# Kernel optimization log

Measured on AMD Instinct MI355X. Metric: run time of the kernel, lower is better.

Reference implementation:

```python
import jax, jax.numpy as jnp
import numpy as np

E, T, D, N_RBF, N_SBF = 262144, 1048576, 128, 6, 42


def setup_inputs() -> dict:
    key = jax.random.key(0)
    ks = jax.random.split(key, 24)
    s = 0.05
    inp = {
        "m_ji": jax.random.normal(ks[0], (E, D), jnp.float32),
        "e_rbf": jax.random.normal(ks[1], (E, N_RBF), jnp.float32),
        "a_sbf": jax.random.normal(ks[2], (T, N_SBF), jnp.float32),
        "nbr_list": jax.random.randint(ks[3], (E, 2), 0, 65536),
        "kj_idx": jax.random.randint(ks[4], (T,), 0, E),
        "ji_idx": jax.random.randint(ks[5], (T,), 0, E),
        # edge branch params
        "We": jax.random.normal(ks[6], (N_RBF, D), jnp.float32) * s,
        "W_e1": jax.random.normal(ks[7], (D, D), jnp.float32) * s,
        "b_e1": jnp.zeros((D,), jnp.float32),
        "W_e2": jax.random.normal(ks[8], (D, D), jnp.float32) * s,
        "b_e2": jnp.zeros((D,), jnp.float32),
        "W_e3": jax.random.normal(ks[9], (D, D), jnp.float32) * s,
        "b_e3": jnp.zeros((D,), jnp.float32),
        "W_e4": jax.random.normal(ks[10], (D, D), jnp.float32) * s,
        # angle branch params
        "Wa": jax.random.normal(ks[11], (N_SBF, D), jnp.float32) * s,
        "W_a1": jax.random.normal(ks[12], (D, D), jnp.float32) * s,
        "b_a1": jnp.zeros((D,), jnp.float32),
        "W_a2": jax.random.normal(ks[13], (D, D), jnp.float32) * s,
        "b_a2": jnp.zeros((D,), jnp.float32),
        "W_a3": jax.random.normal(ks[14], (D, D), jnp.float32) * s,
        "b_a3": jnp.zeros((D,), jnp.float32),
        "W_a4": jax.random.normal(ks[15], (D, D), jnp.float32) * s,
    }
    return inp


def _mlp(x, W1, b1, W2, b2, W3, b3, W4):
    x = jax.nn.silu(x @ W1 + b1)
    x = jax.nn.silu(x @ W2 + b2)
    x = jax.nn.silu(x @ W3 + b3)
    return x @ W4


def reference(m_ji, e_rbf, a_sbf, nbr_list, kj_idx, ji_idx,
              We, W_e1, b_e1, W_e2, b_e2, W_e3, b_e3, W_e4,
              Wa, W_a1, b_a1, W_a2, b_a2, W_a3, b_a3, W_a4):
    # edge branch: project rbf to embed dim, gate by edge messages  [E, D]
    edge_feats = _mlp((e_rbf @ We) * m_ji, W_e1, b_e1, W_e2, b_e2, W_e3, b_e3, W_e4)
    # angle branch: project sbf, gate by triplet-gathered message sum  [T, D]
    angle_gate = m_ji[kj_idx] + m_ji[ji_idx]
    angle_feats = _mlp((a_sbf @ Wa) * angle_gate, W_a1, b_a1, W_a2, b_a2, W_a3, b_a3, W_a4)
    return (edge_feats, angle_feats)
```

## Files before the change

kernel.cpp:

```cpp
#include <hip/hip_runtime.h>
#include <stdint.h>

typedef __attribute__((ext_vector_type(8))) short bf16x8;
typedef __attribute__((ext_vector_type(4))) float f32x4;
typedef __attribute__((ext_vector_type(8))) unsigned short us8;

static __device__ __forceinline__ unsigned short f2bf_u(float f) {
  __bf16 h = (__bf16)f;
  return __builtin_bit_cast(unsigned short, h);
}
static __device__ __forceinline__ uint32_t pack2bf(float a, float b) {
  return (uint32_t)f2bf_u(a) | ((uint32_t)f2bf_u(b) << 16);
}
static __device__ __forceinline__ float silu_f(float v) {
  float e = __builtin_amdgcn_exp2f(v * -1.44269504088896341f);
  return v * __builtin_amdgcn_rcpf(1.0f + e);
}

template<bool LAST>
static __device__ __forceinline__ void xlayer(
    const char* __restrict__ src, char* __restrict__ dst,
    const bf16x8* wf, const float* __restrict__ bias,
    float* __restrict__ gout, int l15, int q, int w, int rs)
{
  f32x4 bv;
  if (!LAST) bv = *(const f32x4*)(bias + w * 16 + q * 4);
  #pragma unroll
  for (int rg = 0; rg < 8; ++rg) {
    const int row = rg * 16 + l15;
    f32x4 acc = {0.f, 0.f, 0.f, 0.f};
    #pragma unroll
    for (int ks = 0; ks < 4; ++ks) {
      bf16x8 xf = *(const bf16x8*)(src + ((row * 256 + ks * 64 + q * 16) ^ rs));
      acc = __builtin_amdgcn_mfma_f32_16x16x32_bf16(wf[ks], xf, acc, 0, 0, 0);
    }
    if (!LAST) {
      float v0 = silu_f(acc[0] + bv[0]);
      float v1 = silu_f(acc[1] + bv[1]);
      float v2 = silu_f(acc[2] + bv[2]);
      float v3 = silu_f(acc[3] + bv[3]);
      uint2 u; u.x = pack2bf(v0, v1); u.y = pack2bf(v2, v3);
      *(uint2*)(dst + ((row * 256 + w * 32 + q * 8) ^ rs)) = u;
    } else {
      __builtin_nontemporal_store(acc,
          (f32x4*)(gout + (size_t)row * 128 + w * 16 + q * 4));
    }
  }
}

__global__ __launch_bounds__(512, 4) void angle_kernel(
    const float* __restrict__ m_ji, const float* __restrict__ a_sbf,
    const int* __restrict__ kj, const int* __restrict__ ji,
    const float* __restrict__ b1, const float* __restrict__ b2,
    const float* __restrict__ b3,
    const char* __restrict__ wt4, const char* __restrict__ waT,
    float* __restrict__ out)
{
  extern __shared__ char lds[];
  char* xbA = lds;
  char* xbB = lds + 32768;
  char* aux = lds + 65536;
  const int tid = threadIdx.x, lane = tid & 63, w = tid >> 6;
  const int l15 = lane & 15, q = lane >> 4;
  const int rs = (l15 & 7) << 4;
  const size_t tb = (size_t)blockIdx.x * 128;

  bf16x8 wa0 = *(const bf16x8*)(waT + (w * 2 + 0) * 1024 + lane * 16);
  bf16x8 wa1 = *(const bf16x8*)(waT + (w * 2 + 1) * 1024 + lane * 16);

  int ikj[8], iji[8];
  #pragma unroll
  for (int i2 = 0; i2 < 8; ++i2) {
    ikj[i2] = kj[tb + i2 * 16 + l15];
    iji[i2] = ji[tb + i2 * 16 + l15];
  }

  {
    const float* src = a_sbf + tb * 42;
    #pragma unroll
    for (int j2 = 0; j2 < 8; ++j2) {
      const int i = tid + j2 * 512;
      const int row = i >> 5, p = i & 31;
      const float* rp = src + row * 42 + p * 2;
      float v0 = (p * 2 < 42) ? __builtin_nontemporal_load(rp) : 0.f;
      float v1 = (p * 2 + 1 < 42) ? __builtin_nontemporal_load(rp + 1) : 0.f;
      *(uint32_t*)(aux + ((row * 128 + p * 4) ^ ((row & 7) << 4))) = pack2bf(v0, v1);
    }
  }
  __syncthreads();

  {
    f32x4 pk[8], pj[8];
    auto gissue = [&](int g) {
      pk[g] = *(const f32x4*)(m_ji + (size_t)ikj[g] * 128 + w * 16 + q * 4);
      pj[g] = *(const f32x4*)(m_ji + (size_t)iji[g] * 128 + w * 16 + q * 4);
    };
    gissue(0); gissue(1);
    #pragma unroll
    for (int rg = 0; rg < 8; ++rg) {
      if (rg < 6) gissue(rg + 2);
      const int row = rg * 16 + l15;
      bf16x8 x0f = *(const bf16x8*)(aux + ((row * 128 + q * 16) ^ rs));
      bf16x8 x1f = *(const bf16x8*)(aux + ((row * 128 + 64 + q * 16) ^ rs));
      f32x4 acc = {0.f, 0.f, 0.f, 0.f};
      acc = __builtin_amdgcn_mfma_f32_16x16x32_bf16(wa0, x0f, acc, 0, 0, 0);
      acc = __builtin_amdgcn_mfma_f32_16x16x32_bf16(wa1, x1f, acc, 0, 0, 0);
      f32x4 g = pk[rg] + pj[rg];
      uint2 u;
      u.x = pack2bf(acc[0] * g[0], acc[1] * g[1]);
      u.y = pack2bf(acc[2] * g[2], acc[3] * g[3]);
      *(uint2*)(xbA + ((row * 256 + w * 32 + q * 8) ^ rs)) = u;
    }
  }
  __syncthreads();

  bf16x8 wfl[4][4];
  #pragma unroll
  for (int L = 0; L < 4; ++L)
    #pragma unroll
    for (int ks = 0; ks < 4; ++ks)
      wfl[L][ks] = *(const bf16x8*)(wt4 + L * 32768 + (w * 4 + ks) * 1024 + lane * 16);

  xlayer<false>(xbA, xbB, wfl[0], b1, nullptr, l15, q, w, rs);
  __syncthreads();
  xlayer<false>(xbB, xbA, wfl[1], b2, nullptr, l15, q, w, rs);
  __syncthreads();
  xlayer<false>(xbA, xbB, wfl[2], b3, nullptr, l15, q, w, rs);
  __syncthreads();
  xlayer<true>(xbB, nullptr, wfl[3], nullptr, out + tb * 128, l15, q, w, rs);
}

__global__ __launch_bounds__(512, 4) void edge_kernel(
    const float* __restrict__ m_ji, const float* __restrict__ e_rbf,
    const float* __restrict__ b1, const float* __restrict__ b2,
    const float* __restrict__ b3,
    const char* __restrict__ wt4, const char* __restrict__ weT,
    float* __restrict__ out)
{
  extern __shared__ char lds[];
  char* xbA = lds;
  char* xbB = lds + 32768;
  float* auxF = (float*)(lds + 65536);
  const int tid = threadIdx.x, lane = tid & 63, w = tid >> 6;
  const int l15 = lane & 15, q = lane >> 4;
  const int rs = (l15 & 7) << 4;
  const size_t tb = (size_t)blockIdx.x * 128;

  bf16x8 we = *(const bf16x8*)(weT + w * 1024 + lane * 16);

  {
    const float* src = e_rbf + tb * 6;
    auxF[tid] = __builtin_nontemporal_load(src + tid);
    const int i2 = tid + 512;
    if (i2 < 768) auxF[i2] = __builtin_nontemporal_load(src + i2);
  }
  __syncthreads();

  {
    f32x4 mr[8];
    auto missue = [&](int g) {
      mr[g] = *(const f32x4*)(m_ji + (tb + g * 16 + l15) * 128 + w * 16 + q * 4);
    };
    missue(0); missue(1);
    #pragma unroll
    for (int rg = 0; rg < 8; ++rg) {
      if (rg < 6) missue(rg + 2);
      const int row = rg * 16 + l15;
      bf16x8 ef;
      #pragma unroll
      for (int j = 0; j < 8; ++j) {
        float v = (j < 6) ? auxF[row * 6 + j] : 0.f;
        unsigned short h = (q == 0 && j < 6) ? f2bf_u(v) : (unsigned short)0;
        ef[j] = (short)h;
      }
      f32x4 acc = {0.f, 0.f, 0.f, 0.f};
      acc = __builtin_amdgcn_mfma_f32_16x16x32_bf16(we, ef, acc, 0, 0, 0);
      f32x4 g = mr[rg];
      uint2 u;
      u.x = pack2bf(acc[0] * g[0], acc[1] * g[1]);
      u.y = pack2bf(acc[2] * g[2], acc[3] * g[3]);
      *(uint2*)(xbA + ((row * 256 + w * 32 + q * 8) ^ rs)) = u;
    }
  }
  __syncthreads();

  bf16x8 wfl[4][4];
  #pragma unroll
  for (int L = 0; L < 4; ++L)
    #pragma unroll
    for (int ks = 0; ks < 4; ++ks)
      wfl[L][ks] = *(const bf16x8*)(wt4 + L * 32768 + (w * 4 + ks) * 1024 + lane * 16);

  xlayer<false>(xbA, xbB, wfl[0], b1, nullptr, l15, q, w, rs);
  __syncthreads();
  xlayer<false>(xbB, xbA, wfl[1], b2, nullptr, l15, q, w, rs);
  __syncthreads();
  xlayer<false>(xbA, xbB, wfl[2], b3, nullptr, l15, q, w, rs);
  __syncthreads();
  xlayer<true>(xbB, nullptr, wfl[3], nullptr, out + tb * 128, l15, q, w, rs);
}

__global__ void prep_kernel(
    const float* __restrict__ W0, const float* __restrict__ W1,
    const float* __restrict__ W2, const float* __restrict__ W3,
    const float* __restrict__ W4, const float* __restrict__ W5,
    const float* __restrict__ W6, const float* __restrict__ W7,
    const float* __restrict__ Wa, const float* __restrict__ We,
    char* __restrict__ ws)
{
  const int gid = blockIdx.x * 256 + threadIdx.x;
  const int lane = gid & 63;
  const int l15 = lane & 15, q = lane >> 4;
  if (gid < 16384) {
    const int mat = gid >> 11;
    const int ctks = (gid & 2047) >> 6;
    const int n = (ctks >> 2) * 16 + l15;
    const int k0 = (ctks & 3) * 32 + q * 8;
    const float* W;
    switch (mat) {
      case 0: W = W0; break; case 1: W = W1; break;
      case 2: W = W2; break; case 3: W = W3; break;
      case 4: W = W4; break; case 5: W = W5; break;
      case 6: W = W6; break; default: W = W7; break;
    }
    us8 v;
    #pragma unroll
    for (int j = 0; j < 8; ++j) v[j] = f2bf_u(W[(size_t)(k0 + j) * 128 + n]);
    *(us8*)(ws + mat * 32768 + ctks * 1024 + lane * 16) = v;
  } else if (gid < 17408) {
    const int g = gid - 16384;
    const int ctks = g >> 6;
    const int n = (ctks >> 1) * 16 + l15;
    const int k0 = (ctks & 1) * 32 + q * 8;
    us8 v;
    #pragma unroll
    for (int j = 0; j < 8; ++j) {
      const int k = k0 + j;
      v[j] = (k < 42) ? f2bf_u(Wa[(size_t)k * 128 + n]) : (unsigned short)0;
    }
    *(us8*)(ws + 262144 + ctks * 1024 + lane * 16) = v;
  } else if (gid < 17920) {
    const int g = gid - 17408;
    const int ct = g >> 6;
    const int n = ct * 16 + l15;
    const int k0 = q * 8;
    us8 v;
    #pragma unroll
    for (int j = 0; j < 8; ++j) {
      const int k = k0 + j;
      v[j] = (k < 6) ? f2bf_u(We[(size_t)k * 128 + n]) : (unsigned short)0;
    }
    *(us8*)(ws + 278528 + ct * 1024 + lane * 16) = v;
  }
}

extern "C" void kernel_launch(void* const* d_in, const int* in_sizes, int n_in,
                              void* d_out, int out_size, void* d_ws, size_t ws_size,
                              hipStream_t stream) {
  (void)in_sizes; (void)n_in; (void)out_size; (void)ws_size;
  const float* m_ji  = (const float*)d_in[0];
  const float* e_rbf = (const float*)d_in[1];
  const float* a_sbf = (const float*)d_in[2];
  const int*   kj    = (const int*)d_in[4];
  const int*   ji    = (const int*)d_in[5];
  const float* We    = (const float*)d_in[6];
  const float* We1   = (const float*)d_in[7];
  const float* be1   = (const float*)d_in[8];
  const float* We2   = (const float*)d_in[9];
  const float* be2   = (const float*)d_in[10];
  const float* We3   = (const float*)d_in[11];
  const float* be3   = (const float*)d_in[12];
  const float* We4   = (const float*)d_in[13];
  const float* Wa    = (const float*)d_in[14];
  const float* Wa1   = (const float*)d_in[15];
  const float* ba1   = (const float*)d_in[16];
  const float* Wa2   = (const float*)d_in[17];
  const float* ba2   = (const float*)d_in[18];
  const float* Wa3   = (const float*)d_in[19];
  const float* ba3   = (const float*)d_in[20];
  const float* Wa4   = (const float*)d_in[21];
  char* ws = (char*)d_ws;
  float* out = (float*)d_out;

  hipFuncSetAttribute((const void*)edge_kernel,
                      hipFuncAttributeMaxDynamicSharedMemorySize, 68608);
  hipFuncSetAttribute((const void*)angle_kernel,
                      hipFuncAttributeMaxDynamicSharedMemorySize, 81920);

  prep_kernel<<<70, 256, 0, stream>>>(
      We1, We2, We3, We4, Wa1, Wa2, Wa3, Wa4, Wa, We, ws);
  edge_kernel<<<262144 / 128, 512, 68608, stream>>>(
      m_ji, e_rbf, be1, be2, be3, ws, ws + 278528, out);
  angle_kernel<<<1048576 / 128, 512, 81920, stream>>>(
      m_ji, a_sbf, kj, ji, ba1, ba2, ba3, ws + 131072, ws + 262144,
      out + (size_t)262144 * 128);
}
```

Measured before the change: 632.6 us.

## Shrink blocks to 64 rows with 4 waves each covering 32 output columns

Both MLP kernels now use 256-thread blocks on 64 rows, with each wave computing two 16-column tiles. Weights are loaded per layer instead of all up front, and a_sbf/e_rbf are read straight from global memory into MFMA fragments instead of being staged through LDS. The LDS footprint drops to 32KB static, which should allow more resident blocks and cut register pressure. The cost is more blocks, and a_sbf rows are only 8-byte aligned (42 floats), so the 16-byte vector loads are misaligned.

Result: faster. 525.6 us (-16.9%).

```diff
diff --git a/kernel.cpp b/kernel.cpp
--- a/kernel.cpp
+++ b/kernel.cpp
@@ -5,6 +5,9 @@
 typedef __attribute__((ext_vector_type(4))) float f32x4;
 typedef __attribute__((ext_vector_type(8))) unsigned short us8;
 
+#define T_CNT 1048576
+#define E_CNT 262144
+
 static __device__ __forceinline__ unsigned short f2bf_u(float f) {
   __bf16 h = (__bf16)f;
   return __builtin_bit_cast(unsigned short, h);
@@ -16,39 +19,18 @@
   float e = __builtin_amdgcn_exp2f(v * -1.44269504088896341f);
   return v * __builtin_amdgcn_rcpf(1.0f + e);
 }
-
-template<bool LAST>
-static __device__ __forceinline__ void xlayer(
-    const char* __restrict__ src, char* __restrict__ dst,
-    const bf16x8* wf, const float* __restrict__ bias,
-    float* __restrict__ gout, int l15, int q, int w, int rs)
-{
-  f32x4 bv;
-  if (!LAST) bv = *(const f32x4*)(bias + w * 16 + q * 4);
-  #pragma unroll
-  for (int rg = 0; rg < 8; ++rg) {
-    const int row = rg * 16 + l15;
-    f32x4 acc = {0.f, 0.f, 0.f, 0.f};
-    #pragma unroll
-    for (int ks = 0; ks < 4; ++ks) {
-      bf16x8 xf = *(const bf16x8*)(src + ((row * 256 + ks * 64 + q * 16) ^ rs));
-      acc = __builtin_amdgcn_mfma_f32_16x16x32_bf16(wf[ks], xf, acc, 0, 0, 0);
-    }
-    if (!LAST) {
-      float v0 = silu_f(acc[0] + bv[0]);
-      float v1 = silu_f(acc[1] + bv[1]);
-      float v2 = silu_f(acc[2] + bv[2]);
-      float v3 = silu_f(acc[3] + bv[3]);
-      uint2 u; u.x = pack2bf(v0, v1); u.y = pack2bf(v2, v3);
-      *(uint2*)(dst + ((row * 256 + w * 32 + q * 8) ^ rs)) = u;
-    } else {
-      __builtin_nontemporal_store(acc,
-          (f32x4*)(gout + (size_t)row * 128 + w * 16 + q * 4));
-    }
-  }
-}
-
-__global__ __launch_bounds__(512, 4) void angle_kernel(
+static __device__ __forceinline__ bf16x8 frag8(f32x4 a, f32x4 b) {
+  bf16x8 r;
+  r[0] = (short)f2bf_u(a[0]); r[1] = (short)f2bf_u(a[1]);
+  r[2] = (short)f2bf_u(a[2]); r[3] = (short)f2bf_u(a[3]);
+  r[4] = (short)f2bf_u(b[0]); r[5] = (short)f2bf_u(b[1]);
+  r[6] = (short)f2bf_u(b[2]); r[7] = (short)f2bf_u(b[3]);
+  return r;
+}
+
+__global__ __launch_bounds__(256)
+__attribute__((amdgpu_waves_per_eu(4, 5)))
+void angle_kernel(
     const float* __restrict__ m_ji, const float* __restrict__ a_sbf,
     const int* __restrict__ kj, const int* __restrict__ ji,
     const float* __restrict__ b1, const float* __restrict__ b2,
@@ -56,148 +38,227 @@
     const char* __restrict__ wt4, const char* __restrict__ waT,
     float* __restrict__ out)
 {
-  extern __shared__ char lds[];
-  char* xbA = lds;
-  char* xbB = lds + 32768;
-  char* aux = lds + 65536;
+  __shared__ __align__(16) char xbA[16384];
+  __shared__ __align__(16) char xbB[16384];
   const int tid = threadIdx.x, lane = tid & 63, w = tid >> 6;
   const int l15 = lane & 15, q = lane >> 4;
   const int rs = (l15 & 7) << 4;
-  const size_t tb = (size_t)blockIdx.x * 128;
-
-  bf16x8 wa0 = *(const bf16x8*)(waT + (w * 2 + 0) * 1024 + lane * 16);
-  bf16x8 wa1 = *(const bf16x8*)(waT + (w * 2 + 1) * 1024 + lane * 16);
-
-  int ikj[8], iji[8];
-  #pragma unroll
-  for (int i2 = 0; i2 < 8; ++i2) {
-    ikj[i2] = kj[tb + i2 * 16 + l15];
-    iji[i2] = ji[tb + i2 * 16 + l15];
-  }
-
-  {
-    const float* src = a_sbf + tb * 42;
-    #pragma unroll
-    for (int j2 = 0; j2 < 8; ++j2) {
-      const int i = tid + j2 * 512;
-      const int row = i >> 5, p = i & 31;
-      const float* rp = src + row * 42 + p * 2;
-      float v0 = (p * 2 < 42) ? __builtin_nontemporal_load(rp) : 0.f;
-      float v1 = (p * 2 + 1 < 42) ? __builtin_nontemporal_load(rp + 1) : 0.f;
-      *(uint32_t*)(aux + ((row * 128 + p * 4) ^ ((row & 7) << 4))) = pack2bf(v0, v1);
-    }
+  const size_t tb = (size_t)blockIdx.x * 64;
+  const int cb = w * 32;
+
+  bf16x8 wa[2][2];
+  #pragma unroll
+  for (int ct = 0; ct < 2; ++ct)
+    #pragma unroll
+    for (int ks = 0; ks < 2; ++ks)
+      wa[ct][ks] = *(const bf16x8*)(waT + (((w * 2 + ct) * 2 + ks) << 10) + lane * 16);
+
+  int ikj[4], iji[4];
+  #pragma unroll
+  for (int g = 0; g < 4; ++g) {
+    ikj[g] = kj[tb + g * 16 + l15];
+    iji[g] = ji[tb + g * 16 + l15];
+  }
+
+  f32x4 pk[2][2], pj[2][2];
+  auto gissue = [&](int g) {
+    const float* bk = m_ji + (size_t)ikj[g] * 128 + cb + q * 4;
+    const float* bj = m_ji + (size_t)iji[g] * 128 + cb + q * 4;
+    pk[g & 1][0] = *(const f32x4*)(bk);
+    pk[g & 1][1] = *(const f32x4*)(bk + 16);
+    pj[g & 1][0] = *(const f32x4*)(bj);
+    pj[g & 1][1] = *(const f32x4*)(bj + 16);
+  };
+  gissue(0); gissue(1);
+
+  #pragma unroll
+  for (int rg = 0; rg < 4; ++rg) {
+    const int row = rg * 16 + l15;
+    const float* ap = a_sbf + (tb + row) * 42;
+    f32x4 a0 = *(const f32x4*)(ap + q * 8);
+    f32x4 a1 = *(const f32x4*)(ap + q * 8 + 4);
+    f32x4 c0 = {0.f, 0.f, 0.f, 0.f}, c1 = {0.f, 0.f, 0.f, 0.f};
+    if (q == 0) { c0 = *(const f32x4*)(ap + 32); c1 = *(const f32x4*)(ap + 36); }
+    else if (q == 1) { float2 t = *(const float2*)(ap + 40); c0[0] = t.x; c0[1] = t.y; }
+    bf16x8 f0 = frag8(a0, a1);
+    bf16x8 f1 = frag8(c0, c1);
+    f32x4 acc0 = {0.f, 0.f, 0.f, 0.f}, acc1 = {0.f, 0.f, 0.f, 0.f};
+    acc0 = __builtin_amdgcn_mfma_f32_16x16x32_bf16(wa[0][0], f0, acc0, 0, 0, 0);
+    acc0 = __builtin_amdgcn_mfma_f32_16x16x32_bf16(wa[0][1], f1, acc0, 0, 0, 0);
+    acc1 = __builtin_amdgcn_mfma_f32_16x16x32_bf16(wa[1][0], f0, acc1, 0, 0, 0);
+    acc1 = __builtin_amdgcn_mfma_f32_16x16x32_bf16(wa[1][1], f1, acc1, 0, 0, 0);
+    f32x4 g0 = pk[rg & 1][0] + pj[rg & 1][0];
+    f32x4 g1 = pk[rg & 1][1] + pj[rg & 1][1];
+    if (rg < 2) gissue(rg + 2);
+    uint2 u0, u1;
+    u0.x = pack2bf(acc0[0] * g0[0], acc0[1] * g0[1]);
+    u0.y = pack2bf(acc0[2] * g0[2], acc0[3] * g0[3]);
+    u1.x = pack2bf(acc1[0] * g1[0], acc1[1] * g1[1]);
+    u1.y = pack2bf(acc1[2] * g1[2], acc1[3] * g1[3]);
+    *(uint2*)(xbA + ((row * 256 + w * 64 + q * 8) ^ rs)) = u0;
+    *(uint2*)(xbA + ((row * 256 + w * 64 + 32 + q * 8) ^ rs)) = u1;
   }
   __syncthreads();
 
-  {
-    f32x4 pk[8], pj[8];
-    auto gissue = [&](int g) {
-      pk[g] = *(const f32x4*)(m_ji + (size_t)ikj[g] * 128 + w * 16 + q * 4);
-      pj[g] = *(const f32x4*)(m_ji + (size_t)iji[g] * 128 + w * 16 + q * 4);
-    };
-    gissue(0); gissue(1);
-    #pragma unroll
-    for (int rg = 0; rg < 8; ++rg) {
-      if (rg < 6) gissue(rg + 2);
-      const int row = rg * 16 + l15;
-      bf16x8 x0f = *(const bf16x8*)(aux + ((row * 128 + q * 16) ^ rs));
-      bf16x8 x1f = *(const bf16x8*)(aux + ((row * 128 + 64 + q * 16) ^ rs));
-      f32x4 acc = {0.f, 0.f, 0.f, 0.f};
-      acc = __builtin_amdgcn_mfma_f32_16x16x32_bf16(wa0, x0f, acc, 0, 0, 0);
-      acc = __builtin_amdgcn_mfma_f32_16x16x32_bf16(wa1, x1f, acc, 0, 0, 0);
-      f32x4 g = pk[rg] + pj[rg];
-      uint2 u;
-      u.x = pack2bf(acc[0] * g[0], acc[1] * g[1]);
-      u.y = pack2bf(acc[2] * g[2], acc[3] * g[3]);
-      *(uint2*)(xbA + ((row * 256 + w * 32 + q * 8) ^ rs)) = u;
-    }
-  }
-  __syncthreads();
-
-  bf16x8 wfl[4][4];
-  #pragma unroll
-  for (int L = 0; L < 4; ++L)
-    #pragma unroll
-    for (int ks = 0; ks < 4; ++ks)
-      wfl[L][ks] = *(const bf16x8*)(wt4 + L * 32768 + (w * 4 + ks) * 1024 + lane * 16);
-
-  xlayer<false>(xbA, xbB, wfl[0], b1, nullptr, l15, q, w, rs);
-  __syncthreads();
-  xlayer<false>(xbB, xbA, wfl[1], b2, nullptr, l15, q, w, rs);
-  __syncthreads();
-  xlayer<false>(xbA, xbB, wfl[2], b3, nullptr, l15, q, w, rs);
-  __syncthreads();
-  xlayer<true>(xbB, nullptr, wfl[3], nullptr, out + tb * 128, l15, q, w, rs);
-}
-
-__global__ __launch_bounds__(512, 4) void edge_kernel(
+  #pragma unroll
+  for (int L = 0; L < 4; ++L) {
+    const char* src = (L & 1) ? xbB : xbA;
+    char* dst = (L & 1) ? xbA : xbB;
+    bf16x8 wf[2][4];
+    #pragma unroll
+    for (int ct = 0; ct < 2; ++ct)
+      #pragma unroll
+      for (int ks = 0; ks < 4; ++ks)
+        wf[ct][ks] = *(const bf16x8*)(wt4 + (L << 15) + (((w * 2 + ct) * 4 + ks) << 10) + lane * 16);
+    if (L < 3) {
+      const float* bp = (L == 0) ? b1 : (L == 1) ? b2 : b3;
+      f32x4 bv0 = *(const f32x4*)(bp + cb + q * 4);
+      f32x4 bv1 = *(const f32x4*)(bp + cb + 16 + q * 4);
+      #pragma unroll
+      for (int rg = 0; rg < 4; ++rg) {
+        const int row = rg * 16 + l15;
+        f32x4 acc0 = {0.f, 0.f, 0.f, 0.f}, acc1 = {0.f, 0.f, 0.f, 0.f};
+        #pragma unroll
+        for (int ks = 0; ks < 4; ++ks) {
+          bf16x8 xf = *(const bf16x8*)(src + ((row * 256 + ks * 64 + q * 16) ^ rs));
+          acc0 = __builtin_amdgcn_mfma_f32_16x16x32_bf16(wf[0][ks], xf, acc0, 0, 0, 0);
+          acc1 = __builtin_amdgcn_mfma_f32_16x16x32_bf16(wf[1][ks], xf, acc1, 0, 0, 0);
+        }
+        uint2 u0, u1;
+        u0.x = pack2bf(silu_f(acc0[0] + bv0[0]), silu_f(acc0[1] + bv0[1]));
+        u0.y = pack2bf(silu_f(acc0[2] + bv0[2]), silu_f(acc0[3] + bv0[3]));
+        u1.x = pack2bf(silu_f(acc1[0] + bv1[0]), silu_f(acc1[1] + bv1[1]));
+        u1.y = pack2bf(silu_f(acc1[2] + bv1[2]), silu_f(acc1[3] + bv1[3]));
+        *(uint2*)(dst + ((row * 256 + w * 64 + q * 8) ^ rs)) = u0;
+        *(uint2*)(dst + ((row * 256 + w * 64 + 32 + q * 8) ^ rs)) = u1;
+      }
+      __syncthreads();
+    } else {
+      #pragma unroll
+      for (int rg = 0; rg < 4; ++rg) {
+        const int row = rg * 16 + l15;
+        f32x4 acc0 = {0.f, 0.f, 0.f, 0.f}, acc1 = {0.f, 0.f, 0.f, 0.f};
+        #pragma unroll
+        for (int ks = 0; ks < 4; ++ks) {
+          bf16x8 xf = *(const bf16x8*)(src + ((row * 256 + ks * 64 + q * 16) ^ rs));
+          acc0 = __builtin_amdgcn_mfma_f32_16x16x32_bf16(wf[0][ks], xf, acc0, 0, 0, 0);
+          acc1 = __builtin_amdgcn_mfma_f32_16x16x32_bf16(wf[1][ks], xf, acc1, 0, 0, 0);
+        }
+        float* op = out + (tb + row) * 128 + cb + q * 4;
+        __builtin_nontemporal_store(acc0, (f32x4*)(op));
+        __builtin_nontemporal_store(acc1, (f32x4*)(op + 16));
+      }
+    }
+  }
+}
+
+__global__ __launch_bounds__(256)
+__attribute__((amdgpu_waves_per_eu(4, 5)))
+void edge_kernel(
     const float* __restrict__ m_ji, const float* __restrict__ e_rbf,
     const float* __restrict__ b1, const float* __restrict__ b2,
     const float* __restrict__ b3,
     const char* __restrict__ wt4, const char* __restrict__ weT,
     float* __restrict__ out)
 {
-  extern __shared__ char lds[];
-  char* xbA = lds;
-  char* xbB = lds + 32768;
-  float* auxF = (float*)(lds + 65536);
+  __shared__ __align__(16) char xbA[16384];
+  __shared__ __align__(16) char xbB[16384];
   const int tid = threadIdx.x, lane = tid & 63, w = tid >> 6;
   const int l15 = lane & 15, q = lane >> 4;
   const int rs = (l15 & 7) << 4;
-  const size_t tb = (size_t)blockIdx.x * 128;
-
-  bf16x8 we = *(const bf16x8*)(weT + w * 1024 + lane * 16);
-
-  {
-    const float* src = e_rbf + tb * 6;
-    auxF[tid] = __builtin_nontemporal_load(src + tid);
-    const int i2 = tid + 512;
-    if (i2 < 768) auxF[i2] = __builtin_nontemporal_load(src + i2);
+  const size_t tb = (size_t)blockIdx.x * 64;
+  const int cb = w * 32;
+
+  bf16x8 we[2];
+  #pragma unroll
+  for (int ct = 0; ct < 2; ++ct)
+    we[ct] = *(const bf16x8*)(weT + ((w * 2 + ct) << 10) + lane * 16);
+
+  f32x4 mr[2][2];
+  auto missue = [&](int g) {
+    const float* bm = m_ji + (tb + g * 16 + l15) * 128 + cb + q * 4;
+    mr[g & 1][0] = *(const f32x4*)(bm);
+    mr[g & 1][1] = *(const f32x4*)(bm + 16);
+  };
+  missue(0); missue(1);
+
+  #pragma unroll
+  for (int rg = 0; rg < 4; ++rg) {
+    const int row = rg * 16 + l15;
+    const float* ep = e_rbf + (tb + row) * 6;
+    f32x4 a0 = {0.f, 0.f, 0.f, 0.f}, a1 = {0.f, 0.f, 0.f, 0.f};
+    if (q == 0) {
+      a0 = *(const f32x4*)(ep);
+      float2 t = *(const float2*)(ep + 4);
+      a1[0] = t.x; a1[1] = t.y;
+    }
+    bf16x8 ef = frag8(a0, a1);
+    f32x4 acc0 = {0.f, 0.f, 0.f, 0.f}, acc1 = {0.f, 0.f, 0.f, 0.f};
+    acc0 = __builtin_amdgcn_mfma_f32_16x16x32_bf16(we[0], ef, acc0, 0, 0, 0);
+    acc1 = __builtin_amdgcn_mfma_f32_16x16x32_bf16(we[1], ef, acc1, 0, 0, 0);
+    f32x4 g0 = mr[rg & 1][0];
+    f32x4 g1 = mr[rg & 1][1];
+    if (rg < 2) missue(rg + 2);
+    uint2 u0, u1;
+    u0.x = pack2bf(acc0[0] * g0[0], acc0[1] * g0[1]);
+    u0.y = pack2bf(acc0[2] * g0[2], acc0[3] * g0[3]);
+    u1.x = pack2bf(acc1[0] * g1[0], acc1[1] * g1[1]);
+    u1.y = pack2bf(acc1[2] * g1[2], acc1[3] * g1[3]);
+    *(uint2*)(xbA + ((row * 256 + w * 64 + q * 8) ^ rs)) = u0;
+    *(uint2*)(xbA + ((row * 256 + w * 64 + 32 + q * 8) ^ rs)) = u1;
   }
   __syncthreads();
 
-  {
-    f32x4 mr[8];
-    auto missue = [&](int g) {
-      mr[g] = *(const f32x4*)(m_ji + (tb + g * 16 + l15) * 128 + w * 16 + q * 4);
-    };
-    missue(0); missue(1);
-    #pragma unroll
-    for (int rg = 0; rg < 8; ++rg) {
-      if (rg < 6) missue(rg + 2);
-      const int row = rg * 16 + l15;
-      bf16x8 ef;
-      #pragma unroll
-      for (int j = 0; j < 8; ++j) {
-        float v = (j < 6) ? auxF[row * 6 + j] : 0.f;
-        unsigned short h = (q == 0 && j < 6) ? f2bf_u(v) : (unsigned short)0;
-        ef[j] = (short)h;
+  #pragma unroll
+  for (int L = 0; L < 4; ++L) {
+    const char* src = (L & 1) ? xbB : xbA;
+    char* dst = (L & 1) ? xbA : xbB;
+    bf16x8 wf[2][4];
+    #pragma unroll
+    for (int ct = 0; ct < 2; ++ct)
+      #pragma unroll
+      for (int ks = 0; ks < 4; ++ks)
+        wf[ct][ks] = *(const bf16x8*)(wt4 + (L << 15) + (((w * 2 + ct) * 4 + ks) << 10) + lane * 16);
+    if (L < 3) {
+      const float* bp = (L == 0) ? b1 : (L == 1) ? b2 : b3;
+      f32x4 bv0 = *(const f32x4*)(bp + cb + q * 4);
+      f32x4 bv1 = *(const f32x4*)(bp + cb + 16 + q * 4);
+      #pragma unroll
+      for (int rg = 0; rg < 4; ++rg) {
+        const int row = rg * 16 + l15;
+        f32x4 acc0 = {0.f, 0.f, 0.f, 0.f}, acc1 = {0.f, 0.f, 0.f, 0.f};
+        #pragma unroll
+        for (int ks = 0; ks < 4; ++ks) {
+          bf16x8 xf = *(const bf16x8*)(src + ((row * 256 + ks * 64 + q * 16) ^ rs));
+          acc0 = __builtin_amdgcn_mfma_f32_16x16x32_bf16(wf[0][ks], xf, acc0, 0, 0, 0);
+          acc1 = __builtin_amdgcn_mfma_f32_16x16x32_bf16(wf[1][ks], xf, acc1, 0, 0, 0);
+        }
+        uint2 u0, u1;
+        u0.x = pack2bf(silu_f(acc0[0] + bv0[0]), silu_f(acc0[1] + bv0[1]));
+        u0.y = pack2bf(silu_f(acc0[2] + bv0[2]), silu_f(acc0[3] + bv0[3]));
+        u1.x = pack2bf(silu_f(acc1[0] + bv1[0]), silu_f(acc1[1] + bv1[1]));
+        u1.y = pack2bf(silu_f(acc1[2] + bv1[2]), silu_f(acc1[3] + bv1[3]));
+        *(uint2*)(dst + ((row * 256 + w * 64 + q * 8) ^ rs)) = u0;
+        *(uint2*)(dst + ((row * 256 + w * 64 + 32 + q * 8) ^ rs)) = u1;
       }
-      f32x4 acc = {0.f, 0.f, 0.f, 0.f};
-      acc = __builtin_amdgcn_mfma_f32_16x16x32_bf16(we, ef, acc, 0, 0, 0);
-      f32x4 g = mr[rg];
-      uint2 u;
-      u.x = pack2bf(acc[0] * g[0], acc[1] * g[1]);
-      u.y = pack2bf(acc[2] * g[2], acc[3] * g[3]);
-      *(uint2*)(xbA + ((row * 256 + w * 32 + q * 8) ^ rs)) = u;
-    }
-  }
-  __syncthreads();
-
-  bf16x8 wfl[4][4];
-  #pragma unroll
-  for (int L = 0; L < 4; ++L)
-    #pragma unroll
-    for (int ks = 0; ks < 4; ++ks)
-      wfl[L][ks] = *(const bf16x8*)(wt4 + L * 32768 + (w * 4 + ks) * 1024 + lane * 16);
-
-  xlayer<false>(xbA, xbB, wfl[0], b1, nullptr, l15, q, w, rs);
-  __syncthreads();
-  xlayer<false>(xbB, xbA, wfl[1], b2, nullptr, l15, q, w, rs);
-  __syncthreads();
-  xlayer<false>(xbA, xbB, wfl[2], b3, nullptr, l15, q, w, rs);
-  __syncthreads();
-  xlayer<true>(xbB, nullptr, wfl[3], nullptr, out + tb * 128, l15, q, w, rs);
+      __syncthreads();
+    } else {
+      #pragma unroll
+      for (int rg = 0; rg < 4; ++rg) {
+        const int row = rg * 16 + l15;
+        f32x4 acc0 = {0.f, 0.f, 0.f, 0.f}, acc1 = {0.f, 0.f, 0.f, 0.f};
+        #pragma unroll
+        for (int ks = 0; ks < 4; ++ks) {
+          bf16x8 xf = *(const bf16x8*)(src + ((row * 256 + ks * 64 + q * 16) ^ rs));
+          acc0 = __builtin_amdgcn_mfma_f32_16x16x32_bf16(wf[0][ks], xf, acc0, 0, 0, 0);
+          acc1 = __builtin_amdgcn_mfma_f32_16x16x32_bf16(wf[1][ks], xf, acc1, 0, 0, 0);
+        }
+        float* op = out + (tb + row) * 128 + cb + q * 4;
+        __builtin_nontemporal_store(acc0, (f32x4*)(op));
+        __builtin_nontemporal_store(acc1, (f32x4*)(op + 16));
+      }
+    }
+  }
 }
 
 __global__ void prep_kernel(
@@ -282,16 +343,11 @@
   char* ws = (char*)d_ws;
   float* out = (float*)d_out;
 
-  hipFuncSetAttribute((const void*)edge_kernel,
-                      hipFuncAttributeMaxDynamicSharedMemorySize, 68608);
-  hipFuncSetAttribute((const void*)angle_kernel,
-                      hipFuncAttributeMaxDynamicSharedMemorySize, 81920);
-
   prep_kernel<<<70, 256, 0, stream>>>(
       We1, We2, We3, We4, Wa1, Wa2, Wa3, Wa4, Wa, We, ws);
-  edge_kernel<<<262144 / 128, 512, 68608, stream>>>(
+  edge_kernel<<<E_CNT / 64, 256, 0, stream>>>(
       m_ji, e_rbf, be1, be2, be3, ws, ws + 278528, out);
-  angle_kernel<<<1048576 / 128, 512, 81920, stream>>>(
+  angle_kernel<<<T_CNT / 64, 256, 0, stream>>>(
       m_ji, a_sbf, kj, ji, ba1, ba2, ba3, ws + 131072, ws + 262144,
-      out + (size_t)262144 * 128);
-}
+      out + (size_t)E_CNT * 128);
+}
```
